# Performance work log

Measured on AMD Instinct MI355X. Metric: run time of the kernel, lower is better.

## Reference

```python
import jax, jax.numpy as jnp
import numpy as np

B, T, C = 4, 2048, 2048
H = 16
D = C // H  # 128


def setup_inputs() -> dict:
    key = jax.random.key(0)
    k1, k2, k3, k4 = jax.random.split(key, 4)
    x = jax.random.normal(k1, (B, T, C), dtype=jnp.float32)
    rope_freqs = jax.random.uniform(k2, (D // 2,), dtype=jnp.float32)
    # torch Linear weights: (out_features, in_features)
    W_attn = jax.random.normal(k3, (3 * C, C), dtype=jnp.float32) * (1.0 / np.sqrt(C))
    W_proj = jax.random.normal(k4, (C, C), dtype=jnp.float32) * (1.0 / np.sqrt(C))
    return {"x": x, "rope_freqs": rope_freqs, "W_attn": W_attn, "W_proj": W_proj}


def _apply_rope(q, k, rope_freqs):
    # q, k: (B, H, T, D); rope_freqs: (D//2,)
    S = q.shape[2]
    positions = jnp.arange(S, dtype=q.dtype)[:, None]            # (S, 1)
    theta = positions * rope_freqs[None, :]                       # (S, D//2)
    sin_t = jnp.sin(theta)[None, None]                            # (1,1,S,D//2)
    cos_t = jnp.cos(theta)[None, None]
    q1, q2 = q[..., 0::2], q[..., 1::2]
    k1, k2 = k[..., 0::2], k[..., 1::2]
    q_out = jnp.concatenate([q1 * cos_t - q2 * sin_t, q1 * sin_t + q2 * cos_t], axis=-1)
    k_out = jnp.concatenate([k1 * cos_t - k2 * sin_t, k1 * sin_t + k2 * cos_t], axis=-1)
    return q_out, k_out


def reference(x, rope_freqs, W_attn, W_proj):
    b, t, c = x.shape
    qkv = jnp.einsum('btc,fc->btf', x, W_attn)                    # (B,T,3C)
    q, k, v = jnp.split(qkv, 3, axis=-1)
    q = q.reshape(b, t, H, D).transpose(0, 2, 1, 3)               # (B,H,T,D)
    k = k.reshape(b, t, H, D).transpose(0, 2, 1, 3)
    v = v.reshape(b, t, H, D).transpose(0, 2, 1, 3)
    q, k = _apply_rope(q, k, rope_freqs)
    scale = 1.0 / jnp.sqrt(jnp.asarray(D, dtype=x.dtype))
    scores = jnp.einsum('bhqd,bhkd->bhqk', q, k) * scale          # (B,H,T,T)
    causal = jnp.tril(jnp.ones((t, t), dtype=bool))
    scores = jnp.where(causal[None, None], scores, jnp.asarray(-jnp.inf, dtype=scores.dtype))
    probs = jax.nn.softmax(scores, axis=-1)
    y = jnp.einsum('bhqk,bhkd->bhqd', probs, v)                   # (B,H,T,D)
    y = y.transpose(0, 2, 1, 3).reshape(b, t, c)
    return jnp.einsum('btc,fc->btf', y, W_proj)
```

## Files before the change

kernel.cpp:

```cpp
#include <hip/hip_runtime.h>
#include <cstdint>
#include <cstddef>


typedef unsigned short u16;
typedef u16    u16x8 __attribute__((ext_vector_type(8)));
typedef __bf16 bf16x8 __attribute__((ext_vector_type(8)));
typedef float  f32x4 __attribute__((ext_vector_type(4)));

#define MFMA16(a, b, c) __builtin_amdgcn_mfma_f32_16x16x32_bf16( \
    __builtin_bit_cast(bf16x8, (a)), __builtin_bit_cast(bf16x8, (b)), (c), 0, 0, 0)

static __device__ __forceinline__ u16 f2b(float f) {
  unsigned u = __builtin_bit_cast(unsigned, f);
  unsigned r = (u + 0x7FFFu + ((u >> 16) & 1u)) >> 16;
  return (u16)r;
}

static __device__ __forceinline__ void gld_lds16(const void* g, void* l) {
  __builtin_amdgcn_global_load_lds(
      (__attribute__((address_space(1))) unsigned int*)(void*)(g),
      (__attribute__((address_space(3))) unsigned int*)(l),
      16, 0, 0);
}

__global__ __launch_bounds__(256) void cvt_bf16(const float4* __restrict__ src,
                                                u16x8* __restrict__ dst, int n8) {
  int i = blockIdx.x * 256 + threadIdx.x;
  if (i >= n8) return;
  float4 a = src[i * 2], b = src[i * 2 + 1];
  u16x8 o;
  o[0] = f2b(a.x); o[1] = f2b(a.y); o[2] = f2b(a.z); o[3] = f2b(a.w);
  o[4] = f2b(b.x); o[5] = f2b(b.y); o[6] = f2b(b.z); o[7] = f2b(b.w);
  dst[i] = o;
}

__global__ __launch_bounds__(256) void gemm_qkv(
    const u16* __restrict__ A, const u16* __restrict__ Bw,
    const float* __restrict__ freqs, int K,
    u16* __restrict__ Qp, u16* __restrict__ Kp, u16* __restrict__ Vp) {
  __shared__ alignas(16) u16 lA[128 * 64];
  __shared__ alignas(16) u16 lB[128 * 64];
  const int tid = threadIdx.x;
  const int lane = tid & 63, wv = tid >> 6;
  const int quad = lane >> 4, col = lane & 15;
  const int wm = wv & 1, wn = wv >> 1;
  const int m0 = blockIdx.y * 128, n0 = blockIdx.x * 128;

  f32x4 acc[4][4];
#pragma unroll
  for (int i = 0; i < 4; ++i)
#pragma unroll
    for (int j = 0; j < 4; ++j) acc[i][j] = (f32x4){0.f, 0.f, 0.f, 0.f};

  for (int k0 = 0; k0 < K; k0 += 64) {
    __syncthreads();
#pragma unroll
    for (int u = 0; u < 4; ++u) {
      int ci = ((wv * 4 + u) << 6) + lane;
      int m = ci >> 3, c = ci & 7;
      int sc = c ^ (m & 7);
      gld_lds16(A + (size_t)(m0 + m) * K + k0 + (sc << 3), lA + ((size_t)(wv * 4 + u) << 9));
      gld_lds16(Bw + (size_t)(n0 + m) * K + k0 + (sc << 3), lB + ((size_t)(wv * 4 + u) << 9));
    }
    __syncthreads();
#pragma unroll
    for (int t = 0; t < 2; ++t) {
      u16x8 af[4], bf[4];
#pragma unroll
      for (int i = 0; i < 4; ++i) {
        int m = wm * 64 + i * 16 + col;
        af[i] = *(const u16x8*)&lA[(m * 8 + (((t << 2) | quad) ^ (m & 7))) * 8];
        int n = wn * 64 + i * 16 + col;
        bf[i] = *(const u16x8*)&lB[(n * 8 + (((t << 2) | quad) ^ (n & 7))) * 8];
      }
#pragma unroll
      for (int i = 0; i < 4; ++i)
#pragma unroll
        for (int j = 0; j < 4; ++j) acc[i][j] = MFMA16(af[i], bf[j], acc[i][j]);
    }
  }

  const int which = n0 >> 11;
  const int h = (n0 & 2047) >> 7;
  if (which == 2) {
#pragma unroll
    for (int i = 0; i < 4; ++i) {
      int mg = m0 + wm * 64 + i * 16 + quad * 4;
#pragma unroll
      for (int j = 0; j < 4; ++j) {
        int d = wn * 64 + j * 16 + col;
#pragma unroll
        for (int r = 0; r < 4; ++r) {
          int m = mg + r;
          int b = m >> 11, t = m & 2047;
          size_t off = ((((size_t)(b * 16 + h)) * 32 + (size_t)(t >> 6)) * 128 + (size_t)d) * 64
                       + (size_t)(t & 63);
          Vp[off] = f2b(acc[i][j][r]);
        }
      }
    }
  } else {
    u16* dst = (which == 0) ? Qp : Kp;
#pragma unroll
    for (int j = 0; j < 4; ++j) {
      int dd = wn * 64 + j * 16 + col;
      int jj = dd >> 1;
      bool even = (dd & 1) == 0;
      float fr = freqs[jj];
      int dout = even ? jj : jj + 64;
#pragma unroll
      for (int i = 0; i < 4; ++i) {
        int mg = m0 + wm * 64 + i * 16 + quad * 4;
#pragma unroll
        for (int r = 0; r < 4; ++r) {
          float own = acc[i][j][r];
          float par = __shfl_xor(own, 1);
          int m = mg + r;
          int b = m >> 11, t = m & 2047;
          float theta = (float)t * fr;
          float rev = theta * 0.15915494309189535f;
          rev -= floorf(rev);
          float s = __builtin_amdgcn_sinf(rev);
          float c = __builtin_amdgcn_cosf(rev);
          float outv = even ? (own * c - par * s) : (par * s + own * c);
          size_t off = ((((size_t)(b * 16 + h)) << 11 | (size_t)t) << 7) | (size_t)dout;
          dst[off] = f2b(outv);
        }
      }
    }
  }
}

__global__ __launch_bounds__(256) void gemm_proj(
    const u16* __restrict__ A, const u16* __restrict__ Bw,
    int N, int K, float* __restrict__ out) {
  __shared__ alignas(16) u16 lA[128 * 64];
  __shared__ alignas(16) u16 lB[128 * 64];
  const int tid = threadIdx.x;
  const int lane = tid & 63, wv = tid >> 6;
  const int quad = lane >> 4, col = lane & 15;
  const int wm = wv & 1, wn = wv >> 1;
  const int m0 = blockIdx.y * 128, n0 = blockIdx.x * 128;

  f32x4 acc[4][4];
#pragma unroll
  for (int i = 0; i < 4; ++i)
#pragma unroll
    for (int j = 0; j < 4; ++j) acc[i][j] = (f32x4){0.f, 0.f, 0.f, 0.f};

  for (int k0 = 0; k0 < K; k0 += 64) {
    __syncthreads();
#pragma unroll
    for (int u = 0; u < 4; ++u) {
      int ci = ((wv * 4 + u) << 6) + lane;
      int m = ci >> 3, c = ci & 7;
      int sc = c ^ (m & 7);
      gld_lds16(A + (size_t)(m0 + m) * K + k0 + (sc << 3), lA + ((size_t)(wv * 4 + u) << 9));
      gld_lds16(Bw + (size_t)(n0 + m) * K + k0 + (sc << 3), lB + ((size_t)(wv * 4 + u) << 9));
    }
    __syncthreads();
#pragma unroll
    for (int t = 0; t < 2; ++t) {
      u16x8 af[4], bf[4];
#pragma unroll
      for (int i = 0; i < 4; ++i) {
        int m = wm * 64 + i * 16 + col;
        af[i] = *(const u16x8*)&lA[(m * 8 + (((t << 2) | quad) ^ (m & 7))) * 8];
        int n = wn * 64 + i * 16 + col;
        bf[i] = *(const u16x8*)&lB[(n * 8 + (((t << 2) | quad) ^ (n & 7))) * 8];
      }
#pragma unroll
      for (int i = 0; i < 4; ++i)
#pragma unroll
        for (int j = 0; j < 4; ++j) acc[i][j] = MFMA16(af[i], bf[j], acc[i][j]);
    }
  }
#pragma unroll
  for (int i = 0; i < 4; ++i) {
    int mg = m0 + wm * 64 + i * 16 + quad * 4;
#pragma unroll
    for (int j = 0; j < 4; ++j) {
      int ng = n0 + wn * 64 + j * 16 + col;
#pragma unroll
      for (int r = 0; r < 4; ++r) out[(size_t)(mg + r) * N + ng] = acc[i][j][r];
    }
  }
}

__global__ __launch_bounds__(512, 4) void fattn(
    const u16* __restrict__ Qb, const u16* __restrict__ Kb, const u16* __restrict__ Vt,
    u16* __restrict__ Yb) {
  __shared__ alignas(16) u16 lK[64 * 128];
  __shared__ alignas(16) u16 lVt[128 * 64];
  __shared__ alignas(16) u16 lP[8][16 * 64];

  const int tid = threadIdx.x;
  const int lane = tid & 63, wv = tid >> 6;
  const int quad = lane >> 4, col = lane & 15;
  const int bh = blockIdx.x;
  const int p = blockIdx.y;
  const int b = bh >> 4, h = bh & 15;
  const size_t base = (size_t)bh << 18;
  const float kcomb = 0.08838834764831845f * 1.4426950408889634f;

#pragma unroll 1
  for (int phase = 0; phase < 2; ++phase) {
    const int tq = phase ? (15 - p) : p;
    const int qr0 = tq * 128 + wv * 16;
    const int dkt = qr0 >> 6;

    u16x8 qf[4];
#pragma unroll
    for (int t = 0; t < 4; ++t)
      qf[t] = *(const u16x8*)(Qb + base + (size_t)(qr0 + col) * 128 + t * 32 + quad * 8);

    f32x4 mrow = (f32x4){-1e30f, -1e30f, -1e30f, -1e30f};
    f32x4 lrow = (f32x4){0.f, 0.f, 0.f, 0.f};
    f32x4 o[8];
#pragma unroll
    for (int dt = 0; dt < 8; ++dt) o[dt] = (f32x4){0.f, 0.f, 0.f, 0.f};

    const int nkt = 2 * tq + 2;
#pragma unroll 1
    for (int kt = 0; kt < nkt; ++kt) {
      __syncthreads();
      if (wv < 4) {
#pragma unroll
        for (int u = 0; u < 4; ++u) {
          int row = wv * 16 + u * 4 + (lane >> 4);
          int sc = (lane & 15) ^ (row & 15);
          gld_lds16(Kb + base + (size_t)(kt * 64 + row) * 128 + (sc << 3),
                    lK + (size_t)(wv * 16 + u * 4) * 128);
        }
      } else {
        int vw = wv - 4;
        const u16* vbase = Vt + ((size_t)(bh * 32 + kt) << 13);
#pragma unroll
        for (int u = 0; u < 4; ++u) {
          int row = vw * 32 + u * 8 + (lane >> 3);
          int sc = (lane & 7) ^ (row & 7);
          gld_lds16(vbase + (size_t)row * 64 + (sc << 3),
                    lVt + (size_t)(vw * 32 + u * 8) * 64);
        }
      }
      __syncthreads();

      if (kt <= dkt) {
        f32x4 sv[4];
#pragma unroll
        for (int nt = 0; nt < 4; ++nt) {
          f32x4 s = (f32x4){0.f, 0.f, 0.f, 0.f};
#pragma unroll
          for (int t = 0; t < 4; ++t) {
            int krow = nt * 16 + col;
            u16x8 kf = *(const u16x8*)&lK[krow * 128 + ((((t << 2) | quad) ^ (krow & 15)) << 3)];
            s = MFMA16(qf[t], kf, s);
          }
          sv[nt] = s;
        }
#pragma unroll
        for (int nt = 0; nt < 4; ++nt)
#pragma unroll
          for (int r = 0; r < 4; ++r) sv[nt][r] *= kcomb;
        if (kt == dkt) {
#pragma unroll
          for (int nt = 0; nt < 4; ++nt) {
            int cg = kt * 64 + nt * 16 + col;
#pragma unroll
            for (int r = 0; r < 4; ++r)
              if (cg > qr0 + quad * 4 + r) sv[nt][r] = -1e30f;
          }
        }
        f32x4 mx = sv[0];
#pragma unroll
        for (int nt = 1; nt < 4; ++nt)
#pragma unroll
          for (int r = 0; r < 4; ++r) mx[r] = fmaxf(mx[r], sv[nt][r]);
#pragma unroll
        for (int off = 1; off < 16; off <<= 1)
#pragma unroll
          for (int r = 0; r < 4; ++r) mx[r] = fmaxf(mx[r], __shfl_xor(mx[r], off));
        f32x4 alpha;
#pragma unroll
        for (int r = 0; r < 4; ++r) {
          float mn = fmaxf(mrow[r], mx[r]);
          alpha[r] = exp2f(mrow[r] - mn);
          mrow[r] = mn;
        }
        f32x4 ps = (f32x4){0.f, 0.f, 0.f, 0.f};
#pragma unroll
        for (int nt = 0; nt < 4; ++nt)
#pragma unroll
          for (int r = 0; r < 4; ++r) {
            float pe = exp2f(sv[nt][r] - mrow[r]);
            ps[r] += pe;
            int row = quad * 4 + r;
            int ch = ((nt << 1) | (col >> 3)) ^ (row & 7);
            lP[wv][row * 64 + (ch << 3) + (col & 7)] = f2b(pe);
          }
#pragma unroll
        for (int off = 1; off < 16; off <<= 1)
#pragma unroll
          for (int r = 0; r < 4; ++r) ps[r] += __shfl_xor(ps[r], off);
#pragma unroll
        for (int r = 0; r < 4; ++r) lrow[r] = lrow[r] * alpha[r] + ps[r];
#pragma unroll
        for (int dt = 0; dt < 8; ++dt)
#pragma unroll
          for (int r = 0; r < 4; ++r) o[dt][r] *= alpha[r];
#pragma unroll
        for (int t = 0; t < 2; ++t) {
          u16x8 pf = *(const u16x8*)&lP[wv][col * 64 + ((((t << 2) | quad) ^ (col & 7)) << 3)];
#pragma unroll
          for (int dt = 0; dt < 8; ++dt) {
            int drow = dt * 16 + col;
            u16x8 vf = *(const u16x8*)&lVt[drow * 64 + ((((t << 2) | quad) ^ (drow & 7)) << 3)];
            o[dt] = MFMA16(pf, vf, o[dt]);
          }
        }
      }
    }

    f32x4 inv;
#pragma unroll
    for (int r = 0; r < 4; ++r) inv[r] = 1.0f / lrow[r];
#pragma unroll
    for (int dt = 0; dt < 8; ++dt)
#pragma unroll
      for (int r = 0; r < 4; ++r) {
        float y = o[dt][r] * inv[r];
        int q = qr0 + quad * 4 + r;
        Yb[((size_t)(b * 2048 + q)) * 2048 + h * 128 + dt * 16 + col] = f2b(y);
      }
  }
}

extern "C" void kernel_launch(void* const* d_in, const int* in_sizes, int n_in,
                              void* d_out, int out_size, void* d_ws, size_t ws_size,
                              hipStream_t stream) {
  (void)in_sizes; (void)n_in; (void)out_size; (void)ws_size;
  const float* x     = (const float*)d_in[0];
  const float* freqs = (const float*)d_in[1];
  const float* Wattn = (const float*)d_in[2];
  const float* Wproj = (const float*)d_in[3];
  float* out = (float*)d_out;
  char* ws = (char*)d_ws;

  u16* Wq_b = (u16*)(ws + 0);
  u16* Wp_b = (u16*)(ws + 25165824);
  u16* x_b  = (u16*)(ws + 33554432);
  u16* Qb   = (u16*)(ws + 67108864);
  u16* Kb   = (u16*)(ws + 100663296);
  u16* Vt   = (u16*)(ws + 134217728);
  u16* Yb   = (u16*)(ws + 167772160);

  cvt_bf16<<<6144, 256, 0, stream>>>((const float4*)Wattn, (u16x8*)Wq_b, 12582912 / 8);
  cvt_bf16<<<2048, 256, 0, stream>>>((const float4*)Wproj, (u16x8*)Wp_b, 4194304 / 8);
  cvt_bf16<<<8192, 256, 0, stream>>>((const float4*)x, (u16x8*)x_b, 16777216 / 8);

  gemm_qkv<<<dim3(48, 64), 256, 0, stream>>>(x_b, Wq_b, freqs, 2048, Qb, Kb, Vt);
  fattn<<<dim3(64, 8), 512, 0, stream>>>(Qb, Kb, Vt, Yb);
  gemm_proj<<<dim3(16, 64), 256, 0, stream>>>(Yb, Wp_b, 2048, 2048, out);
}
```

Before: 678.2 us.

## Rewrite QKV and projection GEMMs as 256x256 double-buffered pipelined tiles

Measured after the change: 591.0 us. -12.9%, faster.

```diff
diff --git a/kernel.cpp b/kernel.cpp
--- a/kernel.cpp
+++ b/kernel.cpp
@@ -23,6 +23,11 @@
       (__attribute__((address_space(3))) unsigned int*)(l),
       16, 0, 0);
 }
+
+#define BARRIER() asm volatile("s_barrier" ::: "memory")
+#define LGKM0()   do { asm volatile("s_waitcnt lgkmcnt(0)" ::: "memory"); \
+                       __builtin_amdgcn_sched_barrier(0); } while (0)
+#define WAIT_VM(n) asm volatile("s_waitcnt vmcnt(" #n ")" ::: "memory")
 
 __global__ __launch_bounds__(256) void cvt_bf16(const float4* __restrict__ src,
                                                 u16x8* __restrict__ dst, int n8) {
@@ -35,61 +40,168 @@
   dst[i] = o;
 }
 
-__global__ __launch_bounds__(256) void gemm_qkv(
+static __device__ __forceinline__ void rdA(u16x8 (&af)[4][2], const u16* p,
+                                           int cx0, int cx1) {
+#pragma unroll
+  for (int i = 0; i < 4; ++i) {
+    af[i][0] = *(const u16x8*)(p + i * 1024 + cx0);
+    af[i][1] = *(const u16x8*)(p + i * 1024 + cx1);
+  }
+}
+
+static __device__ __forceinline__ void rdB(u16x8 (&bf)[2][2], const u16* p,
+                                           int cx0, int cx1) {
+#pragma unroll
+  for (int j = 0; j < 2; ++j) {
+    bf[j][0] = *(const u16x8*)(p + j * 1024 + cx0);
+    bf[j][1] = *(const u16x8*)(p + j * 1024 + cx1);
+  }
+}
+
+static __device__ __forceinline__ void mm16(f32x4 (&acc)[8][4], int ib, int jb,
+                                            const u16x8 (&af)[4][2],
+                                            const u16x8 (&bf)[2][2]) {
+#pragma unroll
+  for (int i = 0; i < 4; ++i)
+#pragma unroll
+    for (int j = 0; j < 2; ++j) {
+      acc[ib + i][jb + j] = MFMA16(af[i][0], bf[j][0], acc[ib + i][jb + j]);
+      acc[ib + i][jb + j] = MFMA16(af[i][1], bf[j][1], acc[ib + i][jb + j]);
+    }
+}
+
+static __device__ __forceinline__ void gemm256_main(
+    const u16* __restrict__ A, const u16* __restrict__ Bw, int K,
+    int m0, int n0, u16* sm, f32x4 (&acc)[8][4]) {
+  const int tid = threadIdx.x;
+  const int lane = tid & 63, wv = tid >> 6;
+  const int quad = lane >> 4, col = lane & 15;
+  const int wm = wv >> 2, wn = wv & 3;
+
+  u16* LA0 = sm;
+  u16* LB0 = sm + 16384;
+  u16* LA1 = sm + 32768;
+  u16* LB1 = sm + 49152;
+
+#pragma unroll
+  for (int i = 0; i < 8; ++i)
+#pragma unroll
+    for (int j = 0; j < 4; ++j) acc[i][j] = (f32x4){0.f, 0.f, 0.f, 0.f};
+
+  const int r8 = lane >> 3, ch = lane & 7;
+  const int sc8 = (ch ^ r8) << 3;
+  const u16 *aS[4], *bS[4];
+  int dof[4];
+#pragma unroll
+  for (int u = 0; u < 4; ++u) {
+    int row = u * 64 + wv * 8 + r8;
+    aS[u] = A + (size_t)(m0 + row) * K + sc8;
+    bS[u] = Bw + (size_t)(n0 + row) * K + sc8;
+    dof[u] = (u * 64 + wv * 8) * 64;
+  }
+
+  const int cx0 = ((quad) ^ (col & 7)) << 3;
+  const int cx1 = ((4 | quad) ^ (col & 7)) << 3;
+  const int offA = (wm * 128 + col) * 64;
+  const int offB = (wn * 64 + col) * 64;
+
+  gld_lds16(bS[0], LB0 + dof[0]); gld_lds16(bS[1], LB0 + dof[1]);
+  gld_lds16(bS[2], LB0 + dof[2]); gld_lds16(bS[3], LB0 + dof[3]);
+  gld_lds16(aS[0], LA0 + dof[0]); gld_lds16(aS[2], LA0 + dof[2]);
+  gld_lds16(aS[1], LA0 + dof[1]); gld_lds16(aS[3], LA0 + dof[3]);
+  WAIT_VM(2);
+  BARRIER();
+
+  u16x8 af[4][2], bfL[2][2], bfH[2][2];
+  const int nIt = K >> 7;
+#pragma unroll 1
+  for (int it = 0; it < nIt; ++it) {
+    const size_t ko = (size_t)it * 128 + 64;
+    const size_t kn = (size_t)it * 128 + 128;
+    const bool hn = (it + 1 < nIt);
+
+    rdA(af, LA0 + offA, cx0, cx1);
+    rdB(bfL, LB0 + offB, cx0, cx1);
+    gld_lds16(bS[0] + ko, LB1 + dof[0]); gld_lds16(bS[1] + ko, LB1 + dof[1]);
+    BARRIER(); LGKM0();
+    __builtin_amdgcn_s_setprio(1); mm16(acc, 0, 0, af, bfL);
+    __builtin_amdgcn_s_setprio(0);
+    BARRIER();
+    rdB(bfH, LB0 + offB + 2048, cx0, cx1);
+    gld_lds16(bS[2] + ko, LB1 + dof[2]); gld_lds16(bS[3] + ko, LB1 + dof[3]);
+    WAIT_VM(4);
+    BARRIER(); LGKM0();
+    __builtin_amdgcn_s_setprio(1); mm16(acc, 0, 2, af, bfH);
+    __builtin_amdgcn_s_setprio(0);
+    BARRIER();
+    rdA(af, LA0 + offA + 4096, cx0, cx1);
+    gld_lds16(aS[0] + ko, LA1 + dof[0]); gld_lds16(aS[2] + ko, LA1 + dof[2]);
+    BARRIER(); LGKM0();
+    __builtin_amdgcn_s_setprio(1); mm16(acc, 4, 0, af, bfL);
+    __builtin_amdgcn_s_setprio(0);
+    BARRIER();
+    gld_lds16(aS[1] + ko, LA1 + dof[1]); gld_lds16(aS[3] + ko, LA1 + dof[3]);
+    WAIT_VM(2);
+    BARRIER(); __builtin_amdgcn_sched_barrier(0);
+    __builtin_amdgcn_s_setprio(1); mm16(acc, 4, 2, af, bfH);
+    __builtin_amdgcn_s_setprio(0);
+    BARRIER();
+    rdA(af, LA1 + offA, cx0, cx1);
+    rdB(bfL, LB1 + offB, cx0, cx1);
+    if (hn) { gld_lds16(bS[0] + kn, LB0 + dof[0]); gld_lds16(bS[1] + kn, LB0 + dof[1]); }
+    BARRIER(); LGKM0();
+    __builtin_amdgcn_s_setprio(1); mm16(acc, 0, 0, af, bfL);
+    __builtin_amdgcn_s_setprio(0);
+    BARRIER();
+    rdB(bfH, LB1 + offB + 2048, cx0, cx1);
+    if (hn) {
+      gld_lds16(bS[2] + kn, LB0 + dof[2]); gld_lds16(bS[3] + kn, LB0 + dof[3]);
+      WAIT_VM(4);
+    } else {
+      WAIT_VM(0);
+    }
+    BARRIER(); LGKM0();
+    __builtin_amdgcn_s_setprio(1); mm16(acc, 0, 2, af, bfH);
+    __builtin_amdgcn_s_setprio(0);
+    BARRIER();
+    rdA(af, LA1 + offA + 4096, cx0, cx1);
+    if (hn) { gld_lds16(aS[0] + kn, LA0 + dof[0]); gld_lds16(aS[2] + kn, LA0 + dof[2]); }
+    BARRIER(); LGKM0();
+    __builtin_amdgcn_s_setprio(1); mm16(acc, 4, 0, af, bfL);
+    __builtin_amdgcn_s_setprio(0);
+    BARRIER();
+    if (hn) { gld_lds16(aS[1] + kn, LA0 + dof[1]); gld_lds16(aS[3] + kn, LA0 + dof[3]); }
+    WAIT_VM(2);
+    BARRIER(); __builtin_amdgcn_sched_barrier(0);
+    __builtin_amdgcn_s_setprio(1); mm16(acc, 4, 2, af, bfH);
+    __builtin_amdgcn_s_setprio(0);
+    BARRIER();
+  }
+}
+
+__global__ __launch_bounds__(512, 2) void gemm_qkv(
     const u16* __restrict__ A, const u16* __restrict__ Bw,
     const float* __restrict__ freqs, int K,
     u16* __restrict__ Qp, u16* __restrict__ Kp, u16* __restrict__ Vp) {
-  __shared__ alignas(16) u16 lA[128 * 64];
-  __shared__ alignas(16) u16 lB[128 * 64];
+  extern __shared__ u16 sm[];
+  const int m0 = blockIdx.y * 256, n0 = blockIdx.x * 256;
+  f32x4 acc[8][4];
+  gemm256_main(A, Bw, K, m0, n0, sm, acc);
+
   const int tid = threadIdx.x;
   const int lane = tid & 63, wv = tid >> 6;
   const int quad = lane >> 4, col = lane & 15;
-  const int wm = wv & 1, wn = wv >> 1;
-  const int m0 = blockIdx.y * 128, n0 = blockIdx.x * 128;
-
-  f32x4 acc[4][4];
-#pragma unroll
-  for (int i = 0; i < 4; ++i)
-#pragma unroll
-    for (int j = 0; j < 4; ++j) acc[i][j] = (f32x4){0.f, 0.f, 0.f, 0.f};
-
-  for (int k0 = 0; k0 < K; k0 += 64) {
-    __syncthreads();
-#pragma unroll
-    for (int u = 0; u < 4; ++u) {
-      int ci = ((wv * 4 + u) << 6) + lane;
-      int m = ci >> 3, c = ci & 7;
-      int sc = c ^ (m & 7);
-      gld_lds16(A + (size_t)(m0 + m) * K + k0 + (sc << 3), lA + ((size_t)(wv * 4 + u) << 9));
-      gld_lds16(Bw + (size_t)(n0 + m) * K + k0 + (sc << 3), lB + ((size_t)(wv * 4 + u) << 9));
-    }
-    __syncthreads();
-#pragma unroll
-    for (int t = 0; t < 2; ++t) {
-      u16x8 af[4], bf[4];
-#pragma unroll
-      for (int i = 0; i < 4; ++i) {
-        int m = wm * 64 + i * 16 + col;
-        af[i] = *(const u16x8*)&lA[(m * 8 + (((t << 2) | quad) ^ (m & 7))) * 8];
-        int n = wn * 64 + i * 16 + col;
-        bf[i] = *(const u16x8*)&lB[(n * 8 + (((t << 2) | quad) ^ (n & 7))) * 8];
-      }
-#pragma unroll
-      for (int i = 0; i < 4; ++i)
-#pragma unroll
-        for (int j = 0; j < 4; ++j) acc[i][j] = MFMA16(af[i], bf[j], acc[i][j]);
-    }
-  }
+  const int wm = wv >> 2, wn = wv & 3;
 
   const int which = n0 >> 11;
-  const int h = (n0 & 2047) >> 7;
   if (which == 2) {
 #pragma unroll
-    for (int i = 0; i < 4; ++i) {
-      int mg = m0 + wm * 64 + i * 16 + quad * 4;
+    for (int i = 0; i < 8; ++i) {
+      int mg = m0 + wm * 128 + i * 16 + quad * 4;
 #pragma unroll
       for (int j = 0; j < 4; ++j) {
-        int d = wn * 64 + j * 16 + col;
+        int vcol = (n0 + wn * 64 + j * 16 + col) & 2047;
+        int h = vcol >> 7, d = vcol & 127;
 #pragma unroll
         for (int r = 0; r < 4; ++r) {
           int m = mg + r;
@@ -104,14 +216,15 @@
     u16* dst = (which == 0) ? Qp : Kp;
 #pragma unroll
     for (int j = 0; j < 4; ++j) {
-      int dd = wn * 64 + j * 16 + col;
+      int ncol = (n0 + wn * 64 + j * 16 + col) & 2047;
+      int h = ncol >> 7, dd = ncol & 127;
       int jj = dd >> 1;
       bool even = (dd & 1) == 0;
       float fr = freqs[jj];
       int dout = even ? jj : jj + 64;
 #pragma unroll
-      for (int i = 0; i < 4; ++i) {
-        int mg = m0 + wm * 64 + i * 16 + quad * 4;
+      for (int i = 0; i < 8; ++i) {
+        int mg = m0 + wm * 128 + i * 16 + quad * 4;
 #pragma unroll
         for (int r = 0; r < 4; ++r) {
           float own = acc[i][j][r];
@@ -132,53 +245,22 @@
   }
 }
 
-__global__ __launch_bounds__(256) void gemm_proj(
+__global__ __launch_bounds__(512, 2) void gemm_proj(
     const u16* __restrict__ A, const u16* __restrict__ Bw,
     int N, int K, float* __restrict__ out) {
-  __shared__ alignas(16) u16 lA[128 * 64];
-  __shared__ alignas(16) u16 lB[128 * 64];
+  extern __shared__ u16 sm[];
+  const int m0 = blockIdx.y * 256, n0 = blockIdx.x * 256;
+  f32x4 acc[8][4];
+  gemm256_main(A, Bw, K, m0, n0, sm, acc);
+
   const int tid = threadIdx.x;
   const int lane = tid & 63, wv = tid >> 6;
   const int quad = lane >> 4, col = lane & 15;
-  const int wm = wv & 1, wn = wv >> 1;
-  const int m0 = blockIdx.y * 128, n0 = blockIdx.x * 128;
-
-  f32x4 acc[4][4];
-#pragma unroll
-  for (int i = 0; i < 4; ++i)
-#pragma unroll
-    for (int j = 0; j < 4; ++j) acc[i][j] = (f32x4){0.f, 0.f, 0.f, 0.f};
-
-  for (int k0 = 0; k0 < K; k0 += 64) {
-    __syncthreads();
-#pragma unroll
-    for (int u = 0; u < 4; ++u) {
-      int ci = ((wv * 4 + u) << 6) + lane;
-      int m = ci >> 3, c = ci & 7;
-      int sc = c ^ (m & 7);
-      gld_lds16(A + (size_t)(m0 + m) * K + k0 + (sc << 3), lA + ((size_t)(wv * 4 + u) << 9));
-      gld_lds16(Bw + (size_t)(n0 + m) * K + k0 + (sc << 3), lB + ((size_t)(wv * 4 + u) << 9));
-    }
-    __syncthreads();
-#pragma unroll
-    for (int t = 0; t < 2; ++t) {
-      u16x8 af[4], bf[4];
-#pragma unroll
-      for (int i = 0; i < 4; ++i) {
-        int m = wm * 64 + i * 16 + col;
-        af[i] = *(const u16x8*)&lA[(m * 8 + (((t << 2) | quad) ^ (m & 7))) * 8];
-        int n = wn * 64 + i * 16 + col;
-        bf[i] = *(const u16x8*)&lB[(n * 8 + (((t << 2) | quad) ^ (n & 7))) * 8];
-      }
-#pragma unroll
-      for (int i = 0; i < 4; ++i)
-#pragma unroll
-        for (int j = 0; j < 4; ++j) acc[i][j] = MFMA16(af[i], bf[j], acc[i][j]);
-    }
-  }
-#pragma unroll
-  for (int i = 0; i < 4; ++i) {
-    int mg = m0 + wm * 64 + i * 16 + quad * 4;
+  const int wm = wv >> 2, wn = wv & 3;
+
+#pragma unroll
+  for (int i = 0; i < 8; ++i) {
+    int mg = m0 + wm * 128 + i * 16 + quad * 4;
 #pragma unroll
     for (int j = 0; j < 4; ++j) {
       int ng = n0 + wn * 64 + j * 16 + col;
@@ -355,11 +437,20 @@
   u16* Vt   = (u16*)(ws + 134217728);
   u16* Yb   = (u16*)(ws + 167772160);
 
+  static bool attr_done = false;
+  if (!attr_done) {
+    (void)hipFuncSetAttribute((const void*)gemm_qkv,
+                              hipFuncAttributeMaxDynamicSharedMemorySize, 131072);
+    (void)hipFuncSetAttribute((const void*)gemm_proj,
+                              hipFuncAttributeMaxDynamicSharedMemorySize, 131072);
+    attr_done = true;
+  }
+
   cvt_bf16<<<6144, 256, 0, stream>>>((const float4*)Wattn, (u16x8*)Wq_b, 12582912 / 8);
   cvt_bf16<<<2048, 256, 0, stream>>>((const float4*)Wproj, (u16x8*)Wp_b, 4194304 / 8);
   cvt_bf16<<<8192, 256, 0, stream>>>((const float4*)x, (u16x8*)x_b, 16777216 / 8);
 
-  gemm_qkv<<<dim3(48, 64), 256, 0, stream>>>(x_b, Wq_b, freqs, 2048, Qb, Kb, Vt);
+  gemm_qkv<<<dim3(24, 32), 512, 131072, stream>>>(x_b, Wq_b, freqs, 2048, Qb, Kb, Vt);
   fattn<<<dim3(64, 8), 512, 0, stream>>>(Qb, Kb, Vt, Yb);
-  gemm_proj<<<dim3(16, 64), 256, 0, stream>>>(Yb, Wp_b, 2048, 2048, out);
-}
+  gemm_proj<<<dim3(8, 32), 512, 131072, stream>>>(Yb, Wp_b, 2048, 2048, out);
+}
```
